# Performance work log

Measured on AMD Instinct MI355X. Metric: run time of the kernel, lower is better.

## Reference

```python
import jax, jax.numpy as jnp
import numpy as np

B = 4096      # batch
N = 8192      # feature dim (sorted axis)
K_SPARSE = 512


def setup_inputs() -> dict:
    key = jax.random.key(0)
    x = jax.random.normal(key, (B, N), dtype=jnp.float32)
    return {"x": x, "k": K_SPARSE}


def reference(x, k):
    # Train-phase branch of KSparse.call:
    #   kth_smallest = sort(x)[..., N-1-k]  (the (k+1)-th largest value per row)
    #   out = x * (x > kth_smallest[:, None])
    n = x.shape[-1]
    kth = jnp.sort(x, axis=-1)[..., n - 1 - k]          # [B]
    mask = (x > kth[..., None]).astype(x.dtype)          # strictly greater -> keeps top-k
    return x * mask
```

## Files before the change

### kernel.cpp

```cpp
#include <hip/hip_runtime.h>

#define NTHREADS 512
#define N_FEAT   8192
#define NB0      4096
#define SKSZ     (NB0 + NB0 / 8)
#define CAP      2048

typedef float f4v __attribute__((ext_vector_type(4)));

__device__ __forceinline__ unsigned f2k(float f) {
    unsigned u = __float_as_uint(f);
    return u ^ (unsigned)(((int)u >> 31) | 0x80000000);
}
__device__ __forceinline__ float k2f(unsigned kk) {
    return __uint_as_float(kk ^ (unsigned)(((int)(~kk) >> 31) | 0x80000000));
}

__global__ __launch_bounds__(NTHREADS) void ksparse_kernel(
    const float* __restrict__ x, const int* __restrict__ kptr,
    float* __restrict__ out) {

    const int t    = threadIdx.x;
    const int lane = t & 63;
    const int w    = t >> 6;
    const size_t base = (size_t)blockIdx.x * N_FEAT;

    __shared__ unsigned hist[SKSZ];
    __shared__ unsigned cand[CAP];
    __shared__ unsigned ws[8];
    __shared__ unsigned s_bucket, s_r, s_cnt, s_kth;

    const f4v* xv = (const f4v*)(x + base);
    f4v c0 = xv[t], c1 = xv[t + 512], c2 = xv[t + 1024], c3 = xv[t + 1536];

#pragma unroll
    for (int i = 0; i < SKSZ / NTHREADS; ++i) hist[t + i * NTHREADS] = 0u;
    if (t == 0) s_cnt = 0u;
    __syncthreads();

    const unsigned r = (unsigned)kptr[0] + 1u;

    {
        auto h4 = [&](f4v v) {
#pragma unroll
            for (int j = 0; j < 4; ++j) {
                unsigned b = f2k(v[j]) >> 20;
                atomicAdd(&hist[b + (b >> 3)], 1u);
            }
        };
        h4(c0); h4(c1); h4(c2); h4(c3);
    }
    __syncthreads();

    unsigned h[8], sum8 = 0;
#pragma unroll
    for (int j = 0; j < 8; ++j) { h[j] = hist[9 * t + j]; sum8 += h[j]; }
    unsigned S = sum8;
#pragma unroll
    for (int off = 1; off < 64; off <<= 1) {
        unsigned q = (unsigned)__shfl_down((int)S, off, 64);
        if (lane + off < 64) S += q;
    }
    if (lane == 0) ws[w] = S;
    __syncthreads();
    unsigned above = S - sum8;
#pragma unroll
    for (int w2 = 1; w2 < 8; ++w2) if (w2 > w) above += ws[w2];
    if (above < r && above + sum8 >= r) {
        unsigned acc = above;
#pragma unroll
        for (int j = 7; j >= 0; --j) {
            if (acc < r && acc + h[j] >= r) { s_bucket = (unsigned)(8 * t + j); s_r = r - acc; }
            acc += h[j];
        }
    }
    __syncthreads();
    const unsigned bucket = s_bucket;
    const unsigned r2 = s_r;

    {
        auto g4 = [&](f4v v) {
#pragma unroll
            for (int j = 0; j < 4; ++j) {
                unsigned kk = f2k(v[j]);
                if ((kk >> 20) == bucket) {
                    unsigned q = atomicAdd(&s_cnt, 1u);
                    if (q < CAP) cand[q] = kk;
                }
            }
        };
        g4(c0); g4(c1); g4(c2); g4(c3);
    }
    __syncthreads();
    const unsigned m = s_cnt;

    if (m <= CAP) {
        for (unsigned i = t; i < m; i += NTHREADS) {
            unsigned ki = cand[i], g = 0, ge = 0;
            for (unsigned j2 = 0; j2 < m; ++j2) {
                unsigned kj = cand[j2];
                g  += (kj > ki);
                ge += (kj >= ki);
            }
            if (g < r2 && ge >= r2) s_kth = ki;
        }
    } else {
        unsigned prefix = bucket << 20, rk = r2;
        for (int pass = 0; pass < 2; ++pass) {
            const int shift = pass == 0 ? 10 : 0;
            const unsigned hm = pass == 0 ? 0xFFF00000u : 0xFFFFFC00u;
            hist[t] = 0u; hist[t + 512] = 0u;
            __syncthreads();
            auto a4 = [&](f4v v) {
#pragma unroll
                for (int j = 0; j < 4; ++j) {
                    unsigned kk = f2k(v[j]);
                    if ((kk & hm) == prefix) atomicAdd(&hist[(kk >> shift) & 1023u], 1u);
                }
            };
            a4(c0); a4(c1); a4(c2); a4(c3);
            __syncthreads();
            if (t < 64) {
                unsigned C = 0, hh[16];
#pragma unroll
                for (int j2 = 0; j2 < 16; ++j2) { hh[j2] = hist[t * 16 + j2]; C += hh[j2]; }
                unsigned S2 = C;
#pragma unroll
                for (int off = 1; off < 64; off <<= 1) {
                    unsigned q = (unsigned)__shfl_down((int)S2, off, 64);
                    if (lane + off < 64) S2 += q;
                }
                unsigned carry = S2 - C;
                if (S2 >= rk && carry < rk) {
                    unsigned acc = carry;
#pragma unroll
                    for (int j2 = 15; j2 >= 0; --j2) {
                        if (acc < rk && acc + hh[j2] >= rk) { s_bucket = (unsigned)(t * 16 + j2); s_r = rk - acc; }
                        acc += hh[j2];
                    }
                }
            }
            __syncthreads();
            prefix |= s_bucket << shift;
            rk = s_r;
        }
        if (t == 0) s_kth = prefix;
    }
    __syncthreads();
    const float kthf = k2f(s_kth);

    f4v* ov = (f4v*)(out + base);
    {
        auto w4 = [&](f4v v, int idx) {
            f4v o;
#pragma unroll
            for (int j = 0; j < 4; ++j) o[j] = (v[j] > kthf) ? v[j] : 0.0f;
            __builtin_nontemporal_store(o, ov + idx);
        };
        w4(c0, t); w4(c1, t + 512); w4(c2, t + 1024); w4(c3, t + 1536);
    }
}

extern "C" void kernel_launch(void* const* d_in, const int* in_sizes, int n_in,
                              void* d_out, int out_size, void* d_ws, size_t ws_size,
                              hipStream_t stream) {
    const float* x = (const float*)d_in[0];
    const int* k   = (const int*)d_in[1];
    float* out     = (float*)d_out;
    const int B = in_sizes[0] / N_FEAT;
    ksparse_kernel<<<B, NTHREADS, 0, stream>>>(x, k, out);
}
```

Before: 53.80 us.

## Halve block size to 256 threads with 32 elements each and 11-bit radix

Each block now runs 256 threads that each hold eight float4 vectors, instead of 512 threads holding four. The first-level histogram shrinks to 2048 bins on the top 11 key bits, and the candidate buffer shrinks to 1024 entries. The fallback refinement passes are adjusted to match the new bit split. The aim is to cut shared memory and raise occupancy (launch bounds hint of 8 blocks). In exchange, each threshold bucket holds about twice as many candidates, so the quadratic candidate-ranking loop does more work per thread.

```diff
diff --git a/kernel.cpp b/kernel.cpp
--- a/kernel.cpp
+++ b/kernel.cpp
@@ -1,10 +1,11 @@
 #include <hip/hip_runtime.h>
 
-#define NTHREADS 512
+#define NTHREADS 256
 #define N_FEAT   8192
-#define NB0      4096
+#define EPT      32
+#define NB0      2048
 #define SKSZ     (NB0 + NB0 / 8)
-#define CAP      2048
+#define CAP      1024
 
 typedef float f4v __attribute__((ext_vector_type(4)));
 
@@ -16,7 +17,7 @@
     return __uint_as_float(kk ^ (unsigned)(((int)(~kk) >> 31) | 0x80000000));
 }
 
-__global__ __launch_bounds__(NTHREADS) void ksparse_kernel(
+__global__ __launch_bounds__(NTHREADS, 8) void ksparse_kernel(
     const float* __restrict__ x, const int* __restrict__ kptr,
     float* __restrict__ out) {
 
@@ -27,11 +28,13 @@
 
     __shared__ unsigned hist[SKSZ];
     __shared__ unsigned cand[CAP];
-    __shared__ unsigned ws[8];
+    __shared__ unsigned ws[4];
     __shared__ unsigned s_bucket, s_r, s_cnt, s_kth;
 
     const f4v* xv = (const f4v*)(x + base);
-    f4v c0 = xv[t], c1 = xv[t + 512], c2 = xv[t + 1024], c3 = xv[t + 1536];
+    f4v c[8];
+#pragma unroll
+    for (int i = 0; i < 8; ++i) c[i] = xv[t + i * NTHREADS];
 
 #pragma unroll
     for (int i = 0; i < SKSZ / NTHREADS; ++i) hist[t + i * NTHREADS] = 0u;
@@ -40,16 +43,13 @@
 
     const unsigned r = (unsigned)kptr[0] + 1u;
 
-    {
-        auto h4 = [&](f4v v) {
 #pragma unroll
-            for (int j = 0; j < 4; ++j) {
-                unsigned b = f2k(v[j]) >> 20;
-                atomicAdd(&hist[b + (b >> 3)], 1u);
-            }
-        };
-        h4(c0); h4(c1); h4(c2); h4(c3);
-    }
+    for (int i = 0; i < 8; ++i)
+#pragma unroll
+        for (int j = 0; j < 4; ++j) {
+            unsigned b = f2k(c[i][j]) >> 21;
+            atomicAdd(&hist[b + (b >> 3)], 1u);
+        }
     __syncthreads();
 
     unsigned h[8], sum8 = 0;
@@ -65,7 +65,7 @@
     __syncthreads();
     unsigned above = S - sum8;
 #pragma unroll
-    for (int w2 = 1; w2 < 8; ++w2) if (w2 > w) above += ws[w2];
+    for (int w2 = 1; w2 < 4; ++w2) if (w2 > w) above += ws[w2];
     if (above < r && above + sum8 >= r) {
         unsigned acc = above;
 #pragma unroll
@@ -78,19 +78,16 @@
     const unsigned bucket = s_bucket;
     const unsigned r2 = s_r;
 
-    {
-        auto g4 = [&](f4v v) {
 #pragma unroll
-            for (int j = 0; j < 4; ++j) {
-                unsigned kk = f2k(v[j]);
-                if ((kk >> 20) == bucket) {
-                    unsigned q = atomicAdd(&s_cnt, 1u);
-                    if (q < CAP) cand[q] = kk;
-                }
+    for (int i = 0; i < 8; ++i)
+#pragma unroll
+        for (int j = 0; j < 4; ++j) {
+            unsigned kk = f2k(c[i][j]);
+            if ((kk >> 21) == bucket) {
+                unsigned q = atomicAdd(&s_cnt, 1u);
+                if (q < CAP) cand[q] = kk;
             }
-        };
-        g4(c0); g4(c1); g4(c2); g4(c3);
-    }
+        }
     __syncthreads();
     const unsigned m = s_cnt;
 
@@ -105,27 +102,26 @@
             if (g < r2 && ge >= r2) s_kth = ki;
         }
     } else {
-        unsigned prefix = bucket << 20, rk = r2;
+        unsigned prefix = bucket << 21, rk = r2;
+#pragma unroll
         for (int pass = 0; pass < 2; ++pass) {
             const int shift = pass == 0 ? 10 : 0;
-            const unsigned hm = pass == 0 ? 0xFFF00000u : 0xFFFFFC00u;
-            hist[t] = 0u; hist[t + 512] = 0u;
+            const int nb    = pass == 0 ? 2048 : 1024;
+            const unsigned hm = pass == 0 ? 0xFFE00000u : 0xFFFFFC00u;
+            for (int i = 0; i < SKSZ / NTHREADS; ++i) hist[t + i * NTHREADS] = 0u;
             __syncthreads();
-            auto a4 = [&](f4v v) {
-#pragma unroll
+            for (int i = 0; i < 8; ++i)
                 for (int j = 0; j < 4; ++j) {
-                    unsigned kk = f2k(v[j]);
-                    if ((kk & hm) == prefix) atomicAdd(&hist[(kk >> shift) & 1023u], 1u);
+                    unsigned kk = f2k(c[i][j]);
+                    if ((kk & hm) == prefix)
+                        atomicAdd(&hist[(kk >> shift) & (nb - 1)], 1u);
                 }
-            };
-            a4(c0); a4(c1); a4(c2); a4(c3);
             __syncthreads();
             if (t < 64) {
-                unsigned C = 0, hh[16];
-#pragma unroll
-                for (int j2 = 0; j2 < 16; ++j2) { hh[j2] = hist[t * 16 + j2]; C += hh[j2]; }
+                const int per = nb / 64;
+                unsigned C = 0;
+                for (int j2 = 0; j2 < per; ++j2) C += hist[t * per + j2];
                 unsigned S2 = C;
-#pragma unroll
                 for (int off = 1; off < 64; off <<= 1) {
                     unsigned q = (unsigned)__shfl_down((int)S2, off, 64);
                     if (lane + off < 64) S2 += q;
@@ -133,10 +129,10 @@
                 unsigned carry = S2 - C;
                 if (S2 >= rk && carry < rk) {
                     unsigned acc = carry;
-#pragma unroll
-                    for (int j2 = 15; j2 >= 0; --j2) {
-                        if (acc < rk && acc + hh[j2] >= rk) { s_bucket = (unsigned)(t * 16 + j2); s_r = rk - acc; }
-                        acc += hh[j2];
+                    for (int j2 = per - 1; j2 >= 0; --j2) {
+                        unsigned hj = hist[t * per + j2];
+                        if (acc < rk && acc + hj >= rk) { s_bucket = (unsigned)(t * per + j2); s_r = rk - acc; }
+                        acc += hj;
                     }
                 }
             }
@@ -150,14 +146,12 @@
     const float kthf = k2f(s_kth);
 
     f4v* ov = (f4v*)(out + base);
-    {
-        auto w4 = [&](f4v v, int idx) {
-            f4v o;
 #pragma unroll
-            for (int j = 0; j < 4; ++j) o[j] = (v[j] > kthf) ? v[j] : 0.0f;
-            __builtin_nontemporal_store(o, ov + idx);
-        };
-        w4(c0, t); w4(c1, t + 512); w4(c2, t + 1024); w4(c3, t + 1536);
+    for (int i = 0; i < 8; ++i) {
+        f4v o;
+#pragma unroll
+        for (int j = 0; j < 4; ++j) o[j] = (c[i][j] > kthf) ? c[i][j] : 0.0f;
+        __builtin_nontemporal_store(o, ov + t + i * NTHREADS);
     }
 }
 
```

Result: slower. 113.7 us (+111.3%).

## Widen radix histogram to 13 bits and stagger early blocks with sleeps

Applied to the files above, without the earlier changes.

Moves the first-pass histogram from 12 to 13 key bits (8192 buckets with padding every 16), so fewer elements fall into the selected bucket, and cuts the candidate cap to 512. The fallback refinement passes change to 10 and 9 bits to match. The first 1024 blocks also get a block-dependent s_sleep delay to spread out their start, meant to cut contention on the memory system. The trade-offs are more LDS for the histogram (which may lower occupancy), a per-thread scan over 16 buckets, and idle time added to those first blocks.

```diff
diff --git a/kernel.cpp b/kernel.cpp
--- a/kernel.cpp
+++ b/kernel.cpp
@@ -2,9 +2,9 @@
 
 #define NTHREADS 512
 #define N_FEAT   8192
-#define NB0      4096
-#define SKSZ     (NB0 + NB0 / 8)
-#define CAP      2048
+#define NB0      8192
+#define SKSZ     (NB0 + NB0 / 16)
+#define CAP      512
 
 typedef float f4v __attribute__((ext_vector_type(4)));
 
@@ -33,6 +33,12 @@
     const f4v* xv = (const f4v*)(x + base);
     f4v c0 = xv[t], c1 = xv[t + 512], c2 = xv[t + 1024], c3 = xv[t + 1536];
 
+    if (blockIdx.x < 1024) {
+        int stage = (blockIdx.x ^ (blockIdx.x >> 8)) & 3;
+        for (int i = 0; i < stage; ++i)
+            __builtin_amdgcn_s_sleep(100);
+    }
+
 #pragma unroll
     for (int i = 0; i < SKSZ / NTHREADS; ++i) hist[t + i * NTHREADS] = 0u;
     if (t == 0) s_cnt = 0u;
@@ -44,18 +50,18 @@
         auto h4 = [&](f4v v) {
 #pragma unroll
             for (int j = 0; j < 4; ++j) {
-                unsigned b = f2k(v[j]) >> 20;
-                atomicAdd(&hist[b + (b >> 3)], 1u);
+                unsigned b = f2k(v[j]) >> 19;
+                atomicAdd(&hist[b + (b >> 4)], 1u);
             }
         };
         h4(c0); h4(c1); h4(c2); h4(c3);
     }
     __syncthreads();
 
-    unsigned h[8], sum8 = 0;
+    unsigned h[16], sum16 = 0;
 #pragma unroll
-    for (int j = 0; j < 8; ++j) { h[j] = hist[9 * t + j]; sum8 += h[j]; }
-    unsigned S = sum8;
+    for (int j = 0; j < 16; ++j) { h[j] = hist[17 * t + j]; sum16 += h[j]; }
+    unsigned S = sum16;
 #pragma unroll
     for (int off = 1; off < 64; off <<= 1) {
         unsigned q = (unsigned)__shfl_down((int)S, off, 64);
@@ -63,14 +69,14 @@
     }
     if (lane == 0) ws[w] = S;
     __syncthreads();
-    unsigned above = S - sum8;
+    unsigned above = S - sum16;
 #pragma unroll
     for (int w2 = 1; w2 < 8; ++w2) if (w2 > w) above += ws[w2];
-    if (above < r && above + sum8 >= r) {
+    if (above < r && above + sum16 >= r) {
         unsigned acc = above;
 #pragma unroll
-        for (int j = 7; j >= 0; --j) {
-            if (acc < r && acc + h[j] >= r) { s_bucket = (unsigned)(8 * t + j); s_r = r - acc; }
+        for (int j = 15; j >= 0; --j) {
+            if (acc < r && acc + h[j] >= r) { s_bucket = (unsigned)(16 * t + j); s_r = r - acc; }
             acc += h[j];
         }
     }
@@ -83,7 +89,7 @@
 #pragma unroll
             for (int j = 0; j < 4; ++j) {
                 unsigned kk = f2k(v[j]);
-                if ((kk >> 20) == bucket) {
+                if ((kk >> 19) == bucket) {
                     unsigned q = atomicAdd(&s_cnt, 1u);
                     if (q < CAP) cand[q] = kk;
                 }
@@ -105,27 +111,27 @@
             if (g < r2 && ge >= r2) s_kth = ki;
         }
     } else {
-        unsigned prefix = bucket << 20, rk = r2;
+        unsigned prefix = bucket << 19, rk = r2;
         for (int pass = 0; pass < 2; ++pass) {
-            const int shift = pass == 0 ? 10 : 0;
-            const unsigned hm = pass == 0 ? 0xFFF00000u : 0xFFFFFC00u;
+            const int shift = pass == 0 ? 9 : 0;
+            const int nb    = pass == 0 ? 1024 : 512;
+            const unsigned hm = pass == 0 ? 0xFFF80000u : 0xFFFFFE00u;
             hist[t] = 0u; hist[t + 512] = 0u;
             __syncthreads();
             auto a4 = [&](f4v v) {
 #pragma unroll
                 for (int j = 0; j < 4; ++j) {
                     unsigned kk = f2k(v[j]);
-                    if ((kk & hm) == prefix) atomicAdd(&hist[(kk >> shift) & 1023u], 1u);
+                    if ((kk & hm) == prefix) atomicAdd(&hist[(kk >> shift) & (nb - 1)], 1u);
                 }
             };
             a4(c0); a4(c1); a4(c2); a4(c3);
             __syncthreads();
             if (t < 64) {
-                unsigned C = 0, hh[16];
-#pragma unroll
-                for (int j2 = 0; j2 < 16; ++j2) { hh[j2] = hist[t * 16 + j2]; C += hh[j2]; }
+                const int per = nb / 64;
+                unsigned C = 0;
+                for (int j2 = 0; j2 < per; ++j2) C += hist[t * per + j2];
                 unsigned S2 = C;
-#pragma unroll
                 for (int off = 1; off < 64; off <<= 1) {
                     unsigned q = (unsigned)__shfl_down((int)S2, off, 64);
                     if (lane + off < 64) S2 += q;
@@ -133,10 +139,10 @@
                 unsigned carry = S2 - C;
                 if (S2 >= rk && carry < rk) {
                     unsigned acc = carry;
-#pragma unroll
-                    for (int j2 = 15; j2 >= 0; --j2) {
-                        if (acc < rk && acc + hh[j2] >= rk) { s_bucket = (unsigned)(t * 16 + j2); s_r = rk - acc; }
-                        acc += hh[j2];
+                    for (int j2 = per - 1; j2 >= 0; --j2) {
+                        unsigned hj = hist[t * per + j2];
+                        if (acc < rk && acc + hj >= rk) { s_bucket = (unsigned)(t * per + j2); s_r = rk - acc; }
+                        acc += hj;
                     }
                 }
             }
```

Result: slower. 66.31 us (+23.2%).

## Split fused select-and-mask kernel into threshold kernel and apply kernel

Applied to the files above, without the earlier changes.

Splits the single kernel into two. The first computes each row's k-th threshold and stores it in a device global array. The second re-reads x and writes the masked output using 256-thread blocks. This may shorten the select kernel's live ranges and let the store-heavy phase run at its own occupancy. In exchange it reads x a second time (128 MB extra), adds a launch, and the fixed 8192-entry global array caps the batch size.

```diff
diff --git a/kernel.cpp b/kernel.cpp
--- a/kernel.cpp
+++ b/kernel.cpp
@@ -8,6 +8,8 @@
 
 typedef float f4v __attribute__((ext_vector_type(4)));
 
+__device__ float g_thr[8192];
+
 __device__ __forceinline__ unsigned f2k(float f) {
     unsigned u = __float_as_uint(f);
     return u ^ (unsigned)(((int)u >> 31) | 0x80000000);
@@ -16,9 +18,8 @@
     return __uint_as_float(kk ^ (unsigned)(((int)(~kk) >> 31) | 0x80000000));
 }
 
-__global__ __launch_bounds__(NTHREADS) void ksparse_kernel(
-    const float* __restrict__ x, const int* __restrict__ kptr,
-    float* __restrict__ out) {
+__global__ __launch_bounds__(NTHREADS) void select_kernel(
+    const float* __restrict__ x, const int* __restrict__ kptr) {
 
     const int t    = threadIdx.x;
     const int lane = t & 63;
@@ -147,17 +148,29 @@
         if (t == 0) s_kth = prefix;
     }
     __syncthreads();
-    const float kthf = k2f(s_kth);
 
+    if (t == 0) g_thr[blockIdx.x] = k2f(s_kth);
+}
+
+__global__ __launch_bounds__(256) void apply_kernel(
+    const float* __restrict__ x, float* __restrict__ out) {
+
+    const int row = blockIdx.x;
+    const float thr = g_thr[row];
+    const size_t base = (size_t)row * N_FEAT;
+    const f4v* xv = (const f4v*)(x + base);
     f4v* ov = (f4v*)(out + base);
-    {
-        auto w4 = [&](f4v v, int idx) {
-            f4v o;
+    const int t = threadIdx.x;
+
+    f4v v[8];
 #pragma unroll
-            for (int j = 0; j < 4; ++j) o[j] = (v[j] > kthf) ? v[j] : 0.0f;
-            __builtin_nontemporal_store(o, ov + idx);
-        };
-        w4(c0, t); w4(c1, t + 512); w4(c2, t + 1024); w4(c3, t + 1536);
+    for (int i = 0; i < 8; ++i) v[i] = xv[t + i * 256];
+#pragma unroll
+    for (int i = 0; i < 8; ++i) {
+        f4v o;
+#pragma unroll
+        for (int j = 0; j < 4; ++j) o[j] = (v[i][j] > thr) ? v[i][j] : 0.0f;
+        __builtin_nontemporal_store(o, ov + t + i * 256);
     }
 }
 
@@ -168,5 +181,6 @@
     const int* k   = (const int*)d_in[1];
     float* out     = (float*)d_out;
     const int B = in_sizes[0] / N_FEAT;
-    ksparse_kernel<<<B, NTHREADS, 0, stream>>>(x, k, out);
+    select_kernel<<<B, NTHREADS, 0, stream>>>(x, k);
+    apply_kernel<<<B, 256, 0, stream>>>(x, out);
 }
```

Result: slower. 79.42 us (+47.6%).
